# Kernel optimization log

Hardware: AMD Instinct MI355X
Metric: run time of the kernel (lower is better)

Reference implementation:

```python
import jax, jax.numpy as jnp
import numpy as np
from jax import lax

HID = 2048; NK = 16; NV = 32; DK = 128; DV = 128; KSZ = 4; CHUNK = 64; S = 2048
KEY_DIM = NK * DK; VAL_DIM = NV * DV; CONV_DIM = 2 * KEY_DIM + VAL_DIM
EPS = 1e-6


def l2norm(x, eps=1e-6):
    return x * lax.rsqrt((x * x).sum(-1, keepdims=True) + eps)


def chunk_gated_delta_rule(q, k, v, g, beta, chunk=CHUNK):
    # q,k: [B,S,Hv,DK]; v: [B,S,Hv,DV]; g,beta: [B,S,Hv]
    q = l2norm(q); k = l2norm(k)  # use_qk_l2norm_in_kernel=True
    q, k, v = (jnp.swapaxes(x, 1, 2) for x in (q, k, v))  # [B,H,S,D]
    g = jnp.swapaxes(g, 1, 2); beta = jnp.swapaxes(beta, 1, 2)  # [B,H,S]
    B, H, Ssz, Dk = k.shape; Dv = v.shape[-1]
    N = Ssz // chunk  # seq_len chosen divisible by chunk -> pad is no-op
    q = q * (Dk ** -0.5)
    vb = v * beta[..., None]
    kb = k * beta[..., None]
    rs = lambda x: x.reshape(B, H, N, chunk, x.shape[-1])
    q, k, v, kb, vb = map(rs, (q, k, v, kb, vb))
    g = jnp.cumsum(g.reshape(B, H, N, chunk), axis=-1)
    tril = jnp.tril(jnp.ones((chunk, chunk), bool))
    stril = jnp.tril(jnp.ones((chunk, chunk), bool), -1)
    diff = jnp.where(tril, g[..., :, None] - g[..., None, :], 0.0)
    decay_mask = jnp.where(tril, jnp.exp(diff), 0.0)  # [B,H,N,C,C]
    attn = jnp.where(stril, -(kb @ jnp.swapaxes(k, -1, -2)) * decay_mask, 0.0)
    # UT (WY) transform: sequential row updates, scan over in-chunk index
    def ut_body(a, i):
        row = jnp.take(a, i, axis=-2)  # [B,H,N,C]
        new = row + jnp.einsum('bhnk,bhnkj->bhnj', row, a)
        return a.at[:, :, :, i, :].set(new), None
    attn, _ = lax.scan(ut_body, attn, jnp.arange(1, chunk))
    attn = attn + jnp.eye(chunk, dtype=attn.dtype)
    u = attn @ vb                                   # [B,H,N,C,DV]
    kcd = attn @ (kb * jnp.exp(g)[..., None])       # [B,H,N,C,DK]
    init = jnp.zeros((B, H, Dk, Dv), q.dtype)
    def step(state, inp):
        q_i, k_i, u_i, kcd_i, g_i, dm_i = inp
        scores = (q_i @ jnp.swapaxes(k_i, -1, -2)) * dm_i
        v_new = u_i - kcd_i @ state
        inter = (q_i * jnp.exp(g_i)[..., None]) @ state
        o = inter + scores @ v_new
        gl = g_i[..., -1]  # [B,H]
        state = state * jnp.exp(gl)[..., None, None] + jnp.einsum(
            'bhcd,bhce->bhde', k_i * jnp.exp(gl[..., None] - g_i)[..., None], v_new)
        return state, o
    mv = lambda x: jnp.moveaxis(x, 2, 0)
    _, out = lax.scan(step, init, (mv(q), mv(k), mv(u), mv(kcd), mv(g), mv(decay_mask)))
    out = jnp.moveaxis(out, 0, 2).reshape(B, H, Ssz, Dv)
    return jnp.swapaxes(out, 1, 2)  # [B,S,H,DV]


def setup_inputs() -> dict:
    key = jax.random.key(0)
    ks = jax.random.split(key, 8)
    return {
        'hidden_states': jax.random.normal(ks[0], (S, HID), jnp.float32),
        'W_qkv': jax.random.normal(ks[1], (CONV_DIM, HID), jnp.float32) * 0.02,
        'W_z': jax.random.normal(ks[2], (VAL_DIM, HID), jnp.float32) * 0.02,
        'W_a': jax.random.normal(ks[3], (NV, HID), jnp.float32) * 0.02,
        'W_b': jax.random.normal(ks[4], (NV, HID), jnp.float32) * 0.02,
        'conv_w': jax.random.normal(ks[5], (CONV_DIM, 1, KSZ), jnp.float32) * 0.1,
        'dt_bias': jnp.ones((NV,), jnp.float32),
        'A_log': jnp.log(jax.random.uniform(ks[6], (NV,), jnp.float32, 0.1, 16.0)),
        'norm_w': jnp.ones((DV,), jnp.float32),
        'W_out': jax.random.normal(ks[7], (HID, VAL_DIM), jnp.float32) * 0.02,
    }


def reference(hidden_states, W_qkv, W_z, W_a, W_b, conv_w, dt_bias, A_log, norm_w, W_out):
    x = hidden_states  # [S, HID]
    mixed = x @ W_qkv.T  # [S, CONV_DIM]
    z = (x @ W_z.T).reshape(-1, DV)  # [S*NV, DV]
    a = x @ W_a.T  # [S, NV]
    b = x @ W_b.T
    # causal depthwise conv1d (torch pads K-1 both sides then slices [:S])
    conv = lax.conv_general_dilated(
        mixed.T[None], conv_w, (1,), [(KSZ - 1, 0)],
        dimension_numbers=('NCH', 'OIH', 'NCH'), feature_group_count=CONV_DIM)
    mixed = jax.nn.silu(conv[0].T)  # [S, CONV_DIM]
    q = mixed[:, :KEY_DIM].reshape(1, S, NK, DK)
    k = mixed[:, KEY_DIM:2 * KEY_DIM].reshape(1, S, NK, DK)
    v = mixed[:, 2 * KEY_DIM:].reshape(1, S, NV, DV)
    beta = jax.nn.sigmoid(b)[None]  # [1,S,NV]
    g = (-jnp.exp(A_log) * jax.nn.softplus(a + dt_bias))[None]  # [1,S,NV]
    ratio = NV // NK
    q = jnp.repeat(q, ratio, axis=2)
    k = jnp.repeat(k, ratio, axis=2)
    core = chunk_gated_delta_rule(q, k, v, g, beta)  # [1,S,NV,DV]
    h = core.reshape(-1, DV)  # [S*NV, DV]
    var = jnp.mean(h * h, axis=-1, keepdims=True)
    h = h * lax.rsqrt(var + EPS) * norm_w
    h = h * jax.nn.silu(z)
    out = h.reshape(S, VAL_DIM) @ W_out.T  # [S, HID]
    return out
```

## Files before the change

### kernel.cpp

```cpp
#include <hip/hip_runtime.h>
#include <hip/hip_bf16.h>
#include <math.h>

#define S_LEN   2048
#define HIDDIM  2048
#define NKH     16
#define NVH     32
#define DKD     128
#define DVD     128
#define CCH     64
#define NCHK    32
#define KEY_DIM 2048
#define VAL_DIM 4096
#define CONV_DIM 8192

#define PA_LDS_BYTES (16384 + 16384 + 32768 + 4096 + 4096 + 256 + 256 + 256)
#define PB_LDS_BYTES ((8192+8192+4096+8192+2048+1024+1024)*2 + 64*4)
#define G256_LDS_BYTES (3 * 12288 * 2)
#define G128_LDS_BYTES (3 * 8192 * 2)

typedef __bf16 bf16x8 __attribute__((ext_vector_type(8)));
typedef float f32x4 __attribute__((ext_vector_type(4)));

__device__ __forceinline__ float sigmoid_f(float x) { return 1.f / (1.f + __expf(-x)); }
__device__ __forceinline__ float silu_f(float x) { return x * sigmoid_f(x); }
__device__ __forceinline__ ushort f2bf(float f) {
    unsigned u = __float_as_uint(f);
    u += 0x7fffu + ((u >> 16) & 1u);
    return (ushort)(u >> 16);
}
__device__ __forceinline__ float bf2f(ushort u) {
    return __uint_as_float((unsigned)u << 16);
}

#define GLL(srcp, dstp) __builtin_amdgcn_global_load_lds( \
    (const __attribute__((address_space(1))) void*)(srcp), \
    (__attribute__((address_space(3))) void*)(dstp), 16, 0, 0)

__global__ __launch_bounds__(256) void cast_kernel(
    const float* __restrict__ in, ushort* __restrict__ out, int n8)
{
    int t = blockIdx.x * 256 + threadIdx.x;
    if (t >= n8) return;
    float4 v0 = *(const float4*)(in + (size_t)t * 8);
    float4 v1 = *(const float4*)(in + (size_t)t * 8 + 4);
    union { ushort u[8]; uint4 v; } r;
    r.u[0] = f2bf(v0.x); r.u[1] = f2bf(v0.y); r.u[2] = f2bf(v0.z); r.u[3] = f2bf(v0.w);
    r.u[4] = f2bf(v1.x); r.u[5] = f2bf(v1.y); r.u[6] = f2bf(v1.z); r.u[7] = f2bf(v1.w);
    *(uint4*)(out + (size_t)t * 8) = r.v;
}

__global__ __launch_bounds__(256) void cast_ab_kernel(
    const float* __restrict__ Wa, const float* __restrict__ Wb, ushort* __restrict__ out)
{
    int t = blockIdx.x * 256 + threadIdx.x;
    int row = t >> 8;
    int c8 = (t & 255) * 8;
    union { ushort u[8]; uint4 v; } r;
    if (row < 64) {
        const float* src = (row < 32) ? (Wa + (size_t)row * HIDDIM + c8)
                                      : (Wb + (size_t)(row - 32) * HIDDIM + c8);
        float4 v0 = *(const float4*)(src);
        float4 v1 = *(const float4*)(src + 4);
        r.u[0] = f2bf(v0.x); r.u[1] = f2bf(v0.y); r.u[2] = f2bf(v0.z); r.u[3] = f2bf(v0.w);
        r.u[4] = f2bf(v1.x); r.u[5] = f2bf(v1.y); r.u[6] = f2bf(v1.z); r.u[7] = f2bf(v1.w);
    } else {
        r.u[0] = r.u[1] = r.u[2] = r.u[3] = r.u[4] = r.u[5] = r.u[6] = r.u[7] = 0;
    }
    *(uint4*)(out + (size_t)t * 8) = r.v;
}

__global__ __launch_bounds__(512, 2) void gemm256_kernel(
    const ushort* __restrict__ A, const ushort* __restrict__ B,
    float* __restrict__ C0, void* __restrict__ C1,
    int K, int NSPLIT, int ldc0, int ldc1, int c1bf16)
{
    extern __shared__ ushort g2s[];
    const int tid = threadIdx.x;
    const int wv = tid >> 6, ln = tid & 63;
    const int wm = wv >> 2, wn = wv & 3;
    const int lrow = ln & 15, lkg = ln >> 4;
    const int bm = blockIdx.y * 128, bn = blockIdx.x * 256;

    int soffA, soffB[2];
    {
        int l = tid & 63;
        soffA = (((tid >> 6) * 16) + (l & 15)) * K + (l >> 4) * 8;
#pragma unroll
        for (int j = 0; j < 2; ++j) {
            int g = tid + j * 512;
            int lg = g & 63;
            soffB[j] = (((g >> 6) * 16) + (lg & 15)) * K + (lg >> 4) * 8;
        }
    }
    const ushort* Abase = A + (size_t)bm * K;
    const ushort* Bbase = B + (size_t)bn * K;

    f32x4 acc[4][4];
#pragma unroll
    for (int m = 0; m < 4; ++m)
#pragma unroll
        for (int n = 0; n < 4; ++n) {
            f32x4 z = {0.f, 0.f, 0.f, 0.f};
            acc[m][n] = z;
        }

#define G256_STAGE(bb, k0) do {                                            \
        ushort* bufA_ = g2s + (bb) * 12288;                                \
        ushort* bufB_ = bufA_ + 4096;                                      \
        GLL(Abase + soffA + (k0), bufA_ + (wv * 64) * 8);                  \
        _Pragma("unroll")                                                  \
        for (int j_ = 0; j_ < 2; ++j_)                                     \
            GLL(Bbase + soffB[j_] + (k0), bufB_ + (j_ * 512 + wv * 64) * 8);\
    } while (0)

    const int T = K >> 5;
    G256_STAGE(0, 0);
    G256_STAGE(1, 32);
    int bb = 0;
    for (int t = 0; t < T; ++t) {
        if (t + 1 < T) {
            asm volatile("s_waitcnt vmcnt(3)" ::: "memory");
        } else {
            asm volatile("s_waitcnt vmcnt(0)" ::: "memory");
        }
        __builtin_amdgcn_s_barrier();
        if (t + 2 < T) G256_STAGE((bb >= 1) ? (bb - 1) : (bb + 2), (t + 2) * 32);
        const ushort* LA = g2s + bb * 12288;
        const ushort* LB = LA + 4096;
        __builtin_amdgcn_s_setprio(1);
        {
            bf16x8 afv[4], bfv[4];
#pragma unroll
            for (int mf = 0; mf < 4; ++mf)
                afv[mf] = *(const bf16x8*)&LA[((wm * 4 + mf) * 64 + ln) * 8];
#pragma unroll
            for (int nf = 0; nf < 4; ++nf)
                bfv[nf] = *(const bf16x8*)&LB[((wn * 4 + nf) * 64 + ln) * 8];
#pragma unroll
            for (int mf = 0; mf < 4; ++mf)
#pragma unroll
                for (int nf = 0; nf < 4; ++nf)
                    acc[mf][nf] = __builtin_amdgcn_mfma_f32_16x16x32_bf16(
                        afv[mf], bfv[nf], acc[mf][nf], 0, 0, 0);
        }
        __builtin_amdgcn_s_setprio(0);
        bb = (bb == 2) ? 0 : bb + 1;
    }
#undef G256_STAGE

    const bool inC1 = (bn >= NSPLIT);
    const int cboff = bn + wn * 64 - (inC1 ? NSPLIT : 0);
    if (!inC1) {
#pragma unroll
        for (int mf = 0; mf < 4; ++mf) {
            const int row0 = bm + wm * 64 + mf * 16 + lkg * 4;
#pragma unroll
            for (int nf = 0; nf < 4; ++nf) {
                float* cp = C0 + (size_t)row0 * ldc0 + cboff + nf * 16 + lrow;
#pragma unroll
                for (int j = 0; j < 4; ++j) cp[(size_t)j * ldc0] = acc[mf][nf][j];
            }
        }
    } else if (!c1bf16) {
        float* C1f = (float*)C1;
#pragma unroll
        for (int mf = 0; mf < 4; ++mf) {
            const int row0 = bm + wm * 64 + mf * 16 + lkg * 4;
#pragma unroll
            for (int nf = 0; nf < 4; ++nf) {
                float* cp = C1f + (size_t)row0 * ldc1 + cboff + nf * 16 + lrow;
#pragma unroll
                for (int j = 0; j < 4; ++j) cp[(size_t)j * ldc1] = acc[mf][nf][j];
            }
        }
    } else {
        ushort* C1b = (ushort*)C1;
#pragma unroll
        for (int mf = 0; mf < 4; ++mf) {
            const int row0 = bm + wm * 64 + mf * 16 + lkg * 4;
#pragma unroll
            for (int nf = 0; nf < 4; ++nf) {
                ushort* cp = C1b + (size_t)row0 * ldc1 + cboff + nf * 16 + lrow;
#pragma unroll
                for (int j = 0; j < 4; ++j) cp[(size_t)j * ldc1] = f2bf(acc[mf][nf][j]);
            }
        }
    }
}

__global__ __launch_bounds__(256, 2) void gemm128_kernel(
    const ushort* __restrict__ A, const ushort* __restrict__ B,
    float* __restrict__ C, int N, int K)
{
    extern __shared__ ushort g1s[];
    const int tid = threadIdx.x;
    const int wv = tid >> 6, ln = tid & 63;
    const int wm = wv >> 1, wn = wv & 1;
    const int lrow = ln & 15, lkg = ln >> 4;
    const int bm = blockIdx.y * 128, bn = blockIdx.x * 128;

    int soff[2];
#pragma unroll
    for (int j = 0; j < 2; ++j) {
        int g = tid + j * 256;
        int l = g & 63;
        soff[j] = (((g >> 6) * 16) + (l & 15)) * K + (l >> 4) * 8;
    }
    const ushort* Abase = A + (size_t)bm * K;
    const ushort* Bbase = B + (size_t)bn * K;

    f32x4 acc[4][4];
#pragma unroll
    for (int m = 0; m < 4; ++m)
#pragma unroll
        for (int n = 0; n < 4; ++n) {
            f32x4 z = {0.f, 0.f, 0.f, 0.f};
            acc[m][n] = z;
        }

#define G128_STAGE(bb, k0) do {                                            \
        ushort* bufA_ = g1s + (bb) * 8192;                                 \
        ushort* bufB_ = bufA_ + 4096;                                      \
        _Pragma("unroll")                                                  \
        for (int j_ = 0; j_ < 2; ++j_) {                                   \
            GLL(Abase + soff[j_] + (k0), bufA_ + (j_ * 256 + wv * 64) * 8);\
            GLL(Bbase + soff[j_] + (k0), bufB_ + (j_ * 256 + wv * 64) * 8);\
        }                                                                  \
    } while (0)

    const int T = K >> 5;
    G128_STAGE(0, 0);
    G128_STAGE(1, 32);
    int bb = 0;
    for (int t = 0; t < T; ++t) {
        if (t + 1 < T) {
            asm volatile("s_waitcnt vmcnt(4)" ::: "memory");
        } else {
            asm volatile("s_waitcnt vmcnt(0)" ::: "memory");
        }
        __builtin_amdgcn_s_barrier();
        if (t + 2 < T) G128_STAGE((bb >= 1) ? (bb - 1) : (bb + 2), (t + 2) * 32);
        const ushort* LA = g1s + bb * 8192;
        const ushort* LB = LA + 4096;
        __builtin_amdgcn_s_setprio(1);
        {
            bf16x8 afv[4], bfv[4];
#pragma unroll
            for (int mf = 0; mf < 4; ++mf)
                afv[mf] = *(const bf16x8*)&LA[((wm * 4 + mf) * 64 + ln) * 8];
#pragma unroll
            for (int nf = 0; nf < 4; ++nf)
                bfv[nf] = *(const bf16x8*)&LB[((wn * 4 + nf) * 64 + ln) * 8];
#pragma unroll
            for (int mf = 0; mf < 4; ++mf)
#pragma unroll
                for (int nf = 0; nf < 4; ++nf)
                    acc[mf][nf] = __builtin_amdgcn_mfma_f32_16x16x32_bf16(
                        afv[mf], bfv[nf], acc[mf][nf], 0, 0, 0);
        }
        __builtin_amdgcn_s_setprio(0);
        bb = (bb == 2) ? 0 : bb + 1;
    }
#undef G128_STAGE

#pragma unroll
    for (int mf = 0; mf < 4; ++mf) {
        const int row0 = bm + wm * 64 + mf * 16 + lkg * 4;
#pragma unroll
        for (int nf = 0; nf < 4; ++nf) {
            float* cp = C + (size_t)row0 * N + bn + wn * 64 + nf * 16 + lrow;
#pragma unroll
            for (int j = 0; j < 4; ++j) cp[(size_t)j * N] = acc[mf][nf][j];
        }
    }
}

__global__ __launch_bounds__(256) void front_kernel(
    const float* __restrict__ pre, const float* __restrict__ cw,
    ushort* __restrict__ qnb, float* __restrict__ kn, float* __restrict__ vbuf)
{
    __shared__ float stage[4096];
    __shared__ float sums[32];
    __shared__ float scal[32];
    const int s = blockIdx.x;
    const int tid = threadIdx.x;

#pragma unroll
    for (int cg = 0; cg < 8; ++cg) {
        const int c = cg * 1024 + tid * 4;
        float w[4][4];
#pragma unroll
        for (int j = 0; j < 4; ++j) {
            float4 wj = *(const float4*)(cw + (size_t)(c + j) * 4);
            w[j][0] = wj.x; w[j][1] = wj.y; w[j][2] = wj.z; w[j][3] = wj.w;
        }
        float a0 = 0.f, a1 = 0.f, a2 = 0.f, a3 = 0.f;
#pragma unroll
        for (int t = 0; t < 4; ++t) {
            int ss = s - 3 + t;
            if (ss >= 0) {
                float4 x = *(const float4*)(pre + (size_t)ss * CONV_DIM + c);
                a0 = fmaf(x.x, w[0][t], a0);
                a1 = fmaf(x.y, w[1][t], a1);
                a2 = fmaf(x.z, w[2][t], a2);
                a3 = fmaf(x.w, w[3][t], a3);
            }
        }
        a0 = silu_f(a0); a1 = silu_f(a1); a2 = silu_f(a2); a3 = silu_f(a3);
        if (cg < 4) {
            float4 v4 = make_float4(a0, a1, a2, a3);
            *(float4*)&stage[c] = v4;
            float ss2 = a0 * a0 + a1 * a1 + a2 * a2 + a3 * a3;
#pragma unroll
            for (int m = 1; m < 32; m <<= 1) ss2 += __shfl_xor(ss2, m, 32);
            if ((tid & 31) == 0) sums[c >> 7] = ss2;
        } else {
            *(float4*)(vbuf + (size_t)s * VAL_DIM + (c - 4096)) =
                make_float4(a0, a1, a2, a3);
        }
    }
    __syncthreads();
    if (tid < 32) {
        float sc = rsqrtf(sums[tid] + 1e-6f);
        if (tid < 16) sc *= 0.08838834764831843f;
        scal[tid] = sc;
    }
    __syncthreads();
#pragma unroll
    for (int j = 0; j < 4; ++j) {
        const int c = j * 1024 + tid * 4;
        float4 v4 = *(const float4*)&stage[c];
        const float sc = scal[c >> 7];
        v4.x *= sc; v4.y *= sc; v4.z *= sc; v4.w *= sc;
        if (c < 2048) {
            union { ushort u2[4]; uint2 v; } p;
            p.u2[0] = f2bf(v4.x); p.u2[1] = f2bf(v4.y);
            p.u2[2] = f2bf(v4.z); p.u2[3] = f2bf(v4.w);
            *(uint2*)(qnb + ((size_t)(s * NKH + (c >> 7))) * DKD + (c & 127)) = p.v;
        } else {
            *(float4*)(kn + ((size_t)(s * NKH + ((c >> 7) - 16))) * DKD + (c & 127)) = v4;
        }
    }
}

__global__ __launch_bounds__(256) void gb_kernel(
    const float* __restrict__ ab, const float* __restrict__ dt_bias,
    const float* __restrict__ A_log, float* __restrict__ g, float* __restrict__ beta)
{
    int idx = blockIdx.x * 256 + threadIdx.x;
    int s = idx >> 5, h = idx & 31;
    float av = ab[(size_t)s * 128 + h] + dt_bias[h];
    float sp = (av > 20.f) ? av : log1pf(__expf(av));
    g[idx] = -__expf(A_log[h]) * sp;
    beta[idx] = sigmoid_f(ab[(size_t)s * 128 + 32 + h]);
}

__global__ __launch_bounds__(256) void phaseA_kernel(
    const ushort* __restrict__ qnb, const float* __restrict__ kn,
    const float* __restrict__ vbuf, const float* __restrict__ gbuf,
    const float* __restrict__ betabuf,
    float* __restrict__ u, ushort* __restrict__ kcd,
    ushort* __restrict__ scores, float* __restrict__ gcs_out,
    ushort* __restrict__ knT)
{
    extern __shared__ char pasm[];
    ushort* kb    = (ushort*)(pasm);
    ushort* qb    = (ushort*)(pasm + 16384);
    ushort* Xb    = (ushort*)(pasm + 32768);
    float*  Adiag = (float*)(pasm + 65536);
    ushort* Ab    = (ushort*)(pasm + 69632);
    float*  gcs_s = (float*)(pasm + 73728);
    float*  bet_s = (float*)(pasm + 73984);
    float*  scK_s = (float*)(pasm + 74240);
    float*  Pf    = (float*)qb;

    const int n = blockIdx.x, h = blockIdx.y, kh = h >> 1;
    const int tid = threadIdx.x;
    const int s0 = n * CCH;
    const int wv = tid >> 6, ln = tid & 63;
    const int lrow = ln & 15, lkg = ln >> 4;

    float xr[64];
    if (tid < 128) {
        const float* vp = vbuf + (size_t)s0 * VAL_DIM + h * DVD + tid;
#pragma unroll
        for (int i = 0; i < 64; ++i) xr[i] = vp[(size_t)i * VAL_DIM];
    } else {
        const float* kp = kn + ((size_t)s0 * NKH + kh) * DKD + (tid - 128);
#pragma unroll
        for (int i = 0; i < 64; ++i) xr[i] = kp[(size_t)i * (NKH * DKD)];
    }

    {
        uint4 z = {0, 0, 0, 0};
#pragma unroll
        for (int i = 0; i < 8; ++i)
            *(uint4*)&Xb[(i * 256 + tid) * 8] = z;
        *(uint4*)&Ab[tid * 8] = z;
    }

    if (tid < 64) {
        float gv = gbuf[(size_t)(s0 + tid) * NVH + h];
#pragma unroll
        for (int off = 1; off < 64; off <<= 1) {
            float pv = __shfl_up(gv, off, 64);
            if (tid >= off) gv += pv;
        }
        float bv = betabuf[(size_t)(s0 + tid) * NVH + h];
        gcs_s[tid] = gv;
        bet_s[tid] = bv;
        scK_s[tid] = bv * __expf(gv);
        gcs_out[(size_t)h * S_LEN + s0 + tid] = gv;
    }

    {
        const int r = tid >> 2, c0 = (tid & 3) * 32;
        const int mbase = (((r >> 4) * 4 + (tid & 3)) * 64 + (r & 15)) * 8;
        const float* ksrc = kn + ((size_t)(s0 + r) * NKH + kh) * DKD + c0;
#pragma unroll
        for (int j0 = 0; j0 < 4; ++j0) {
            float4 v0 = *(const float4*)(ksrc + j0 * 8);
            float4 v1 = *(const float4*)(ksrc + j0 * 8 + 4);
            union { ushort us[8]; uint4 v; } p;
            p.us[0] = f2bf(v0.x); p.us[1] = f2bf(v0.y); p.us[2] = f2bf(v0.z); p.us[3] = f2bf(v0.w);
            p.us[4] = f2bf(v1.x); p.us[5] = f2bf(v1.y); p.us[6] = f2bf(v1.z); p.us[7] = f2bf(v1.w);
            *(uint4*)&kb[mbase + (j0 << 7)] = p.v;
        }
        const ushort* qsrc = qnb + ((size_t)(s0 + r) * NKH + kh) * DKD + c0;
#pragma unroll
        for (int j0 = 0; j0 < 4; ++j0) {
            uint4 v = *(const uint4*)(qsrc + j0 * 8);
            *(uint4*)&qb[mbase + (j0 << 7)] = v;
        }
    }
    __syncthreads();

    f32x4 accA[4], accQ[4];
#pragma unroll
    for (int j = 0; j < 4; ++j) {
        f32x4 z = {0.f, 0.f, 0.f, 0.f};
        accA[j] = z; accQ[j] = z;
    }
#pragma unroll
    for (int ks = 0; ks < 4; ++ks) {
        bf16x8 a_k = *(const bf16x8*)&kb[((wv * 4 + ks) * 64 + ln) * 8];
        bf16x8 a_q = *(const bf16x8*)&qb[((wv * 4 + ks) * 64 + ln) * 8];
#pragma unroll
        for (int j = 0; j < 4; ++j) {
            bf16x8 b_k = *(const bf16x8*)&kb[((j * 4 + ks) * 64 + ln) * 8];
            accA[j] = __builtin_amdgcn_mfma_f32_16x16x32_bf16(a_k, b_k, accA[j], 0, 0, 0);
            accQ[j] = __builtin_amdgcn_mfma_f32_16x16x32_bf16(a_q, b_k, accQ[j], 0, 0, 0);
        }
    }
    {
        ushort* scp = scores + (size_t)(h * NCHK + n) * (CCH * CCH);
#pragma unroll
        for (int j = 0; j < 4; ++j) {
            const int c = j * 16 + lrow;
            const float gc = gcs_s[c];
#pragma unroll
            for (int jj = 0; jj < 4; ++jj) {
                const int i = wv * 16 + lkg * 4 + jj;
                const float e = __expf(gcs_s[i] - gc);
                float sv = (i >= c) ? (accQ[j][jj] * e) : 0.f;
                scp[i * CCH + c] = f2bf(sv);
                float aval = (i > c) ? (-bet_s[i] * accA[j][jj] * e) : 0.f;
                if (j == wv) {
                    Adiag[wv * 256 + (i & 15) * 16 + lrow] = aval;
                } else if (j < wv) {
                    const int f = (wv == 1) ? 0 : ((wv == 2) ? 1 : (2 + (j >> 1)));
                    const int lk = ((j & 1) << 4) | lrow;
                    const int lane2 = (i & 15) | ((lk >> 3) << 4);
                    Ab[(f * 64 + lane2) * 8 + (lk & 7)] = f2bf(aval);
                }
            }
        }
    }
    if (tid < 128) {
#pragma unroll
        for (int i4 = 0; i4 < 16; ++i4) {
            float4 b4 = *(const float4*)&bet_s[i4 * 4];
            xr[i4 * 4 + 0] *= b4.x; xr[i4 * 4 + 1] *= b4.y;
            xr[i4 * 4 + 2] *= b4.z; xr[i4 * 4 + 3] *= b4.w;
        }
    } else {
#pragma unroll
        for (int i4 = 0; i4 < 16; ++i4) {
            float4 b4 = *(const float4*)&scK_s[i4 * 4];
            xr[i4 * 4 + 0] *= b4.x; xr[i4 * 4 + 1] *= b4.y;
            xr[i4 * 4 + 2] *= b4.z; xr[i4 * 4 + 3] *= b4.w;
        }
    }
    __syncthreads();

    const int ct = tid >> 4, lct = tid & 15;
#pragma unroll
    for (int s = 0; s < 4; ++s) {
        float y[16];
        float pr[16];
        if (s > 0) {
#pragma unroll
            for (int r = 0; r < 16; ++r) pr[r] = Pf[r * 256 + tid];
        } else {
#pragma unroll
            for (int r = 0; r < 16; ++r) pr[r] = 0.f;
        }
#pragma unroll
        for (int r = 0; r < 16; ++r) {
            float acc = xr[s * 16 + r] + pr[r];
#pragma unroll
            for (int k4 = 0; k4 < 16; k4 += 4) {
                if (k4 < r) {
                    float4 a4 = *(const float4*)&Adiag[s * 256 + r * 16 + k4];
                    if (k4 + 0 < r) acc = fmaf(a4.x, y[k4 + 0], acc);
                    if (k4 + 1 < r) acc = fmaf(a4.y, y[k4 + 1], acc);
                    if (k4 + 2 < r) acc = fmaf(a4.z, y[k4 + 2], acc);
                    if (k4 + 3 < r) acc = fmaf(a4.w, y[k4 + 3], acc);
                }
            }
            y[r] = acc;
        }
        if (tid < 128) {
            float* up = u + (size_t)(h * NCHK + n) * (CCH * DVD) + (s * 16) * DVD + tid;
#pragma unroll
            for (int r = 0; r < 16; ++r) up[r * DVD] = y[r];
        } else {
            ushort* kp = kcd + (size_t)(h * NCHK + n) * (CCH * DKD) + (s * 16) * DKD + (tid - 128);
#pragma unroll
            for (int r = 0; r < 16; ++r) kp[r * DKD] = f2bf(y[r]);
        }
        if (s < 3) {
#pragma unroll
            for (int half = 0; half < 2; ++half) {
                union { ushort us[8]; uint4 v; } p;
#pragma unroll
                for (int e = 0; e < 8; ++e) p.us[e] = f2bf(y[half * 8 + e]);
                const int kg = (s & 1) * 2 + half;
                *(uint4*)&Xb[(((s >> 1) * 16 + ct) * 64 + (kg * 16 + lct)) * 8] = p.v;
            }
            __syncthreads();
            const int snx = s + 1;
            const int nT2 = (snx + 1) >> 1;
            f32x4 accP[4];
#pragma unroll
            for (int ctl = 0; ctl < 4; ++ctl) {
                f32x4 z = {0.f, 0.f, 0.f, 0.f};
                accP[ctl] = z;
            }
#pragma unroll
            for (int t2 = 0; t2 < 2; ++t2) {
                if (t2 < nT2) {
                    const int f = (snx == 1) ? 0 : ((snx == 2) ? 1 : (2 + t2));
                    bf16x8 a = *(const bf16x8*)&Ab[(f * 64 + ln) * 8];
#pragma unroll
                    for (int ctl = 0; ctl < 4; ++ctl) {
                        bf16x8 b = *(const bf16x8*)&Xb[((t2 * 16 + wv * 4 + ctl) * 64 + ln) * 8];
                        accP[ctl] = __builtin_amdgcn_mfma_f32_16x16x32_bf16(a, b, accP[ctl], 0, 0, 0);
                    }
                }
            }
#pragma unroll
            for (int ctl = 0; ctl < 4; ++ctl)
#pragma unroll
                for (int jj = 0; jj < 4; ++jj)
                    Pf[(lkg * 4 + jj) * 256 + wv * 64 + ctl * 16 + lrow] = accP[ctl][jj];
            __syncthreads();
        }
    }

    if (!(h & 1)) {
        const int dk = tid >> 1, ch = (tid & 1) * 32;
        ushort* dst = knT + ((size_t)(kh * NCHK + n) * DKD + dk) * CCH + ch;
        const int kpart = ((dk >> 5) * 64) * 8 + (((dk >> 3) & 3) << 4) * 8 + (dk & 7);
#pragma unroll
        for (int j0 = 0; j0 < 32; j0 += 8) {
            union { ushort us[8]; uint4 v; } p;
#pragma unroll
            for (int j = 0; j < 8; ++j) {
                const int row = ch + j0 + j;
                p.us[j] = kb[((row >> 4) * 4 * 64 + (row & 15)) * 8 + kpart];
            }
            *(uint4*)(dst + j0) = p.v;
        }
    }
}

__global__ __launch_bounds__(256) void phaseB_kernel(
    const ushort* __restrict__ qnb, const ushort* __restrict__ knT,
    const float* __restrict__ u, const ushort* __restrict__ kcd,
    const ushort* __restrict__ sc, const float* __restrict__ gcs,
    ushort* __restrict__ obuf)
{
    extern __shared__ ushort smu[];
    ushort* qorg  = smu;
    ushort* kcorg = smu + 8192;
    ushort* scorg = smu + 16384;
    ushort* kTorg = smu + 20480;
    ushort* storg = smu + 28672;
    ushort* vnorg = smu + 30720;
    ushort* vnsorg= smu + 31744;
    float* gcs_s  = (float*)(smu + 32768);

    const int h = blockIdx.x;
    const int dvb = blockIdx.y;
    const int d0 = dvb * 16;
    const int kh = h >> 1;
    const int tid = threadIdx.x;
    const int wv = tid >> 6, ln = tid & 63;
    const int lrow = ln & 15, lkg = ln >> 4;

    for (int i = tid; i < 2048 / 8; i += 256) {
        uint4 z = {0, 0, 0, 0};
        *(uint4*)&storg[i * 8] = z;
    }

    const int q_lane  = lrow * (NKH * DKD) + kh * DKD + wv * 32 + lkg * 8;
    const int kc_lane = lrow * DKD + wv * 32 + lkg * 8;
    const int st_lane = ((tid >> 7) * 16 + lrow) * 64 + ((tid >> 6) & 1) * 32 + lkg * 8;
    const int dst_e   = wv * 512;

    f32x4 accS0 = {0.f, 0.f, 0.f, 0.f}, accS1 = {0.f, 0.f, 0.f, 0.f};

    for (int n = 0; n < NCHK; ++n) {
        const int s0 = n * CCH;
        const ushort* qsrc  = qnb + (size_t)s0 * (NKH * DKD);
        const ushort* kcsrc = kcd + (size_t)(h * NCHK + n) * (CCH * DKD);
        const ushort* scsrc = sc  + (size_t)(h * NCHK + n) * (CCH * CCH);
        const ushort* kTsrc = knT + (size_t)(kh * NCHK + n) * (DKD * CCH);
#pragma unroll
        for (int r = 0; r < 4; ++r) {
            GLL(qsrc + q_lane + r * 32768, &qorg[r * 2048 + dst_e]);
            GLL(kcsrc + kc_lane + r * 2048, &kcorg[r * 2048 + dst_e]);
            GLL(kTsrc + st_lane + r * 2048, &kTorg[r * 2048 + dst_e]);
        }
#pragma unroll
        for (int r = 0; r < 2; ++r)
            GLL(scsrc + st_lane + r * 2048, &scorg[r * 2048 + dst_e]);
        if (tid < 64) gcs_s[tid] = gcs[(size_t)h * S_LEN + s0 + tid];
        __syncthreads();

        f32x4 accv = {0.f, 0.f, 0.f, 0.f};
        f32x4 acco = {0.f, 0.f, 0.f, 0.f};
#pragma unroll
        for (int ks = 0; ks < 4; ++ks) {
            bf16x8 b_st = *(const bf16x8*)&storg[(ks * 64 + ln) * 8];
            bf16x8 a_kc = *(const bf16x8*)&kcorg[((wv * 4 + ks) * 64 + ln) * 8];
            bf16x8 a_q  = *(const bf16x8*)&qorg[((wv * 4 + ks) * 64 + ln) * 8];
            accv = __builtin_amdgcn_mfma_f32_16x16x32_bf16(a_kc, b_st, accv, 0, 0, 0);
            acco = __builtin_amdgcn_mfma_f32_16x16x32_bf16(a_q, b_st, acco, 0, 0, 0);
        }
        const float* up = u + (size_t)(h * NCHK + n) * (CCH * DVD)
                            + (wv * 16 + lkg * 4) * DVD + d0 + lrow;
        float u0 = up[0], u1 = up[DVD], u2 = up[2 * DVD], u3 = up[3 * DVD];
        const float gl = gcs_s[63];
        float vn0 = u0 - accv[0], vn1 = u1 - accv[1];
        float vn2 = u2 - accv[2], vn3 = u3 - accv[3];
        {
            const int row = wv * 16 + lkg * 4;
            float g0 = gcs_s[row], g1 = gcs_s[row + 1], g2 = gcs_s[row + 2], g3 = gcs_s[row + 3];
            acco[0] *= __expf(g0); acco[1] *= __expf(g1);
            acco[2] *= __expf(g2); acco[3] *= __expf(g3);
            const int eb = ((wv >> 1) * 64 + ((wv & 1) * 2 + (lkg >> 1)) * 16 + lrow) * 8
                         + (lkg & 1) * 4;
            union { ushort u2a[4]; uint2 v; } pa, pb;
            pa.u2a[0] = f2bf(vn0); pa.u2a[1] = f2bf(vn1);
            pa.u2a[2] = f2bf(vn2); pa.u2a[3] = f2bf(vn3);
            pb.u2a[0] = f2bf(vn0 * __expf(gl - g0)); pb.u2a[1] = f2bf(vn1 * __expf(gl - g1));
            pb.u2a[2] = f2bf(vn2 * __expf(gl - g2)); pb.u2a[3] = f2bf(vn3 * __expf(gl - g3));
            *(uint2*)&vnorg[eb] = pa.v;
            *(uint2*)&vnsorg[eb] = pb.v;
        }
        __syncthreads();

#pragma unroll
        for (int ks = 0; ks < 2; ++ks) {
            bf16x8 a_sc = *(const bf16x8*)&scorg[((wv * 2 + ks) * 64 + ln) * 8];
            bf16x8 b_vn = *(const bf16x8*)&vnorg[(ks * 64 + ln) * 8];
            acco = __builtin_amdgcn_mfma_f32_16x16x32_bf16(a_sc, b_vn, acco, 0, 0, 0);
        }
        ushort* op = obuf + (size_t)(s0 + wv * 16 + lkg * 4) * VAL_DIM + h * DVD + d0 + lrow;
        op[0] = f2bf(acco[0]); op[VAL_DIM] = f2bf(acco[1]);
        op[2 * VAL_DIM] = f2bf(acco[2]); op[3 * VAL_DIM] = f2bf(acco[3]);

        const float egl = __expf(gl);
        accS0 *= egl; accS1 *= egl;
#pragma unroll
        for (int ks = 0; ks < 2; ++ks) {
            bf16x8 a_vs = *(const bf16x8*)&vnsorg[(ks * 64 + ln) * 8];
            bf16x8 b_k0 = *(const bf16x8*)&kTorg[(((wv * 2 + 0) * 2 + ks) * 64 + ln) * 8];
            bf16x8 b_k1 = *(const bf16x8*)&kTorg[(((wv * 2 + 1) * 2 + ks) * 64 + ln) * 8];
            accS0 = __builtin_amdgcn_mfma_f32_16x16x32_bf16(a_vs, b_k0, accS0, 0, 0, 0);
            accS1 = __builtin_amdgcn_mfma_f32_16x16x32_bf16(a_vs, b_k1, accS1, 0, 0, 0);
        }
#pragma unroll
        for (int j = 0; j < 4; ++j) {
            storg[(wv * 64 + ((lrow >> 3)) * 16 + lkg * 4 + j) * 8 + (lrow & 7)] = f2bf(accS0[j]);
            storg[(wv * 64 + (2 + (lrow >> 3)) * 16 + lkg * 4 + j) * 8 + (lrow & 7)] = f2bf(accS1[j]);
        }
        __syncthreads();
    }
}

__global__ __launch_bounds__(256) void norm_kernel(
    const ushort* __restrict__ obuf, const ushort* __restrict__ z,
    const float* __restrict__ nw, ushort* __restrict__ hbuf)
{
    int row = (blockIdx.x * 256 + threadIdx.x) >> 6;
    int lane = threadIdx.x & 63;
    uint ov = *(const uint*)(obuf + (size_t)row * DVD + lane * 2);
    float x0 = bf2f((ushort)ov), x1 = bf2f((ushort)(ov >> 16));
    float ss = x0 * x0 + x1 * x1;
#pragma unroll
    for (int m = 1; m < 64; m <<= 1) ss += __shfl_xor(ss, m, 64);
    float scale = rsqrtf(ss * (1.f / DVD) + 1e-6f);
    uint zv = *(const uint*)(z + (size_t)row * DVD + lane * 2);
    float z0 = bf2f((ushort)zv), z1 = bf2f((ushort)(zv >> 16));
    float2 w2 = *(const float2*)(nw + lane * 2);
    float h0 = x0 * scale * w2.x * silu_f(z0);
    float h1 = x1 * scale * w2.y * silu_f(z1);
    union { ushort u[2]; uint v; } r;
    r.u[0] = f2bf(h0); r.u[1] = f2bf(h1);
    *(uint*)(hbuf + (size_t)row * DVD + lane * 2) = r.v;
}

extern "C" void kernel_launch(void* const* d_in, const int* in_sizes, int n_in,
                              void* d_out, int out_size, void* d_ws, size_t ws_size,
                              hipStream_t stream)
{
    (void)in_sizes; (void)n_in; (void)out_size; (void)ws_size;
    const float* x      = (const float*)d_in[0];
    const float* W_qkv  = (const float*)d_in[1];
    const float* W_z    = (const float*)d_in[2];
    const float* W_a    = (const float*)d_in[3];
    const float* W_b    = (const float*)d_in[4];
    const float* conv_w = (const float*)d_in[5];
    const float* dt_b   = (const float*)d_in[6];
    const float* A_log  = (const float*)d_in[7];
    const float* norm_w = (const float*)d_in[8];
    const float* W_out  = (const float*)d_in[9];
    float* out = (float*)d_out;

    char* ws = (char*)d_ws;
    float*  mixed_pre = (float*)(ws);
    float*  u_buf     = (float*)(ws);
    ushort* kcd_buf   = (ushort*)(ws + 33554432);
    ushort* knT_buf   = (ushort*)(ws + 50331648);
    ushort* wqz       = (ushort*)(ws + 67108864);
    ushort* xb        = (ushort*)(ws + 117440512);
    float*  vbuf      = (float*)(ws + 67108864);
    ushort* obuf      = (ushort*)(ws + 67108864);
    ushort* hbuf      = (ushort*)(ws + 100663296);
    ushort* wob       = (ushort*)(ws + 117440512);
    ushort* z_buf     = (ushort*)(ws + 134217728);
    ushort* sc_buf    = (ushort*)(ws + 167772160);
    ushort* wabb      = (ushort*)(ws + 167772160);
    float*  ab_buf    = (float*)(ws + 168296448);
    ushort* qnb       = (ushort*)(ws + 176160768);
    float*  kn        = (float*)(ws + 184549376);
    float*  g_buf     = (float*)(ws + 201326592);
    float*  bet_buf   = (float*)(ws + 201588736);
    float*  gcs_buf   = (float*)(ws + 201850880);

    hipFuncSetAttribute((const void*)phaseA_kernel,
                        hipFuncAttributeMaxDynamicSharedMemorySize, PA_LDS_BYTES);
    hipFuncSetAttribute((const void*)phaseB_kernel,
                        hipFuncAttributeMaxDynamicSharedMemorySize, PB_LDS_BYTES);
    hipFuncSetAttribute((const void*)gemm256_kernel,
                        hipFuncAttributeMaxDynamicSharedMemorySize, G256_LDS_BYTES);
    hipFuncSetAttribute((const void*)gemm128_kernel,
                        hipFuncAttributeMaxDynamicSharedMemorySize, G128_LDS_BYTES);

    dim3 blk(256);
    cast_kernel<<<(S_LEN * HIDDIM / 8) / 256, blk, 0, stream>>>(x, xb, S_LEN * HIDDIM / 8);
    cast_kernel<<<(CONV_DIM * HIDDIM / 8) / 256, blk, 0, stream>>>(W_qkv, wqz, CONV_DIM * HIDDIM / 8);
    cast_kernel<<<(VAL_DIM * HIDDIM / 8) / 256, blk, 0, stream>>>(W_z, wqz + (size_t)CONV_DIM * HIDDIM, VAL_DIM * HIDDIM / 8);
    cast_ab_kernel<<<(128 * HIDDIM / 8) / 256, blk, 0, stream>>>(W_a, W_b, wabb);
    gemm256_kernel<<<dim3((CONV_DIM + VAL_DIM) / 256, S_LEN / 128), dim3(512), G256_LDS_BYTES, stream>>>(
        xb, wqz, mixed_pre, (void*)z_buf, HIDDIM, CONV_DIM, CONV_DIM, VAL_DIM, 1);
    gemm128_kernel<<<dim3(1, S_LEN / 128), blk, G128_LDS_BYTES, stream>>>(
        xb, wabb, ab_buf, 128, HIDDIM);
    front_kernel<<<S_LEN, blk, 0, stream>>>(mixed_pre, conv_w, qnb, kn, vbuf);
    gb_kernel<<<(S_LEN * NVH) / 256, blk, 0, stream>>>(ab_buf, dt_b, A_log, g_buf, bet_buf);
    phaseA_kernel<<<dim3(NCHK, NVH), blk, PA_LDS_BYTES, stream>>>(
        qnb, kn, vbuf, g_buf, bet_buf, u_buf, kcd_buf, sc_buf, gcs_buf, knT_buf);
    phaseB_kernel<<<dim3(NVH, 8), blk, PB_LDS_BYTES, stream>>>(
        qnb, knT_buf, u_buf, kcd_buf, sc_buf, gcs_buf, obuf);
    cast_kernel<<<(HIDDIM * VAL_DIM / 8) / 256, blk, 0, stream>>>(W_out, wob, HIDDIM * VAL_DIM / 8);
    norm_kernel<<<(S_LEN * NVH * 64) / 256, blk, 0, stream>>>(obuf, z_buf, norm_w, hbuf);
    gemm128_kernel<<<dim3(HIDDIM / 128, S_LEN / 128), blk, G128_LDS_BYTES, stream>>>(
        hbuf, wob, out, HIDDIM, VAL_DIM);
}
```

Baseline: 478.6 us.

## Double-buffer phaseB chunk loads and store u as bf16 staged in LDS

The sequential phaseB chunk loop gets two LDS buffers, so the global-to-LDS loads for chunk n+1 are issued while chunk n is computed, and the per-chunk load/sync stall goes away. The u intermediate is now written in bf16 instead of fp32, which halves its traffic, and it is staged into LDS with the other operands rather than read directly from global memory. All gcs values for the head are preloaded once. The cost is a much larger LDS footprint per block, which can lower occupancy, plus bf16 rounding of u, which may reduce accuracy.

```diff
diff --git a/kernel.cpp b/kernel.cpp
--- a/kernel.cpp
+++ b/kernel.cpp
@@ -15,7 +15,7 @@
 #define CONV_DIM 8192
 
 #define PA_LDS_BYTES (16384 + 16384 + 32768 + 4096 + 4096 + 256 + 256 + 256)
-#define PB_LDS_BYTES ((8192+8192+4096+8192+2048+1024+1024)*2 + 64*4)
+#define PB_LDS_BYTES ((2 * 29696 + 2048 + 1024 + 1024) * 2 + 2048 * 4)
 #define G256_LDS_BYTES (3 * 12288 * 2)
 #define G128_LDS_BYTES (3 * 8192 * 2)
 
@@ -360,7 +360,7 @@
     const ushort* __restrict__ qnb, const float* __restrict__ kn,
     const float* __restrict__ vbuf, const float* __restrict__ gbuf,
     const float* __restrict__ betabuf,
-    float* __restrict__ u, ushort* __restrict__ kcd,
+    ushort* __restrict__ u, ushort* __restrict__ kcd,
     ushort* __restrict__ scores, float* __restrict__ gcs_out,
     ushort* __restrict__ knT)
 {
@@ -522,9 +522,9 @@
             y[r] = acc;
         }
         if (tid < 128) {
-            float* up = u + (size_t)(h * NCHK + n) * (CCH * DVD) + (s * 16) * DVD + tid;
-#pragma unroll
-            for (int r = 0; r < 16; ++r) up[r * DVD] = y[r];
+            ushort* up = u + (size_t)(h * NCHK + n) * (CCH * DVD) + (s * 16) * DVD + tid;
+#pragma unroll
+            for (int r = 0; r < 16; ++r) up[r * DVD] = f2bf(y[r]);
         } else {
             ushort* kp = kcd + (size_t)(h * NCHK + n) * (CCH * DKD) + (s * 16) * DKD + (tid - 128);
 #pragma unroll
@@ -588,19 +588,15 @@
 
 __global__ __launch_bounds__(256) void phaseB_kernel(
     const ushort* __restrict__ qnb, const ushort* __restrict__ knT,
-    const float* __restrict__ u, const ushort* __restrict__ kcd,
+    const ushort* __restrict__ u, const ushort* __restrict__ kcd,
     const ushort* __restrict__ sc, const float* __restrict__ gcs,
     ushort* __restrict__ obuf)
 {
     extern __shared__ ushort smu[];
-    ushort* qorg  = smu;
-    ushort* kcorg = smu + 8192;
-    ushort* scorg = smu + 16384;
-    ushort* kTorg = smu + 20480;
-    ushort* storg = smu + 28672;
-    ushort* vnorg = smu + 30720;
-    ushort* vnsorg= smu + 31744;
-    float* gcs_s  = (float*)(smu + 32768);
+    ushort* storg  = smu + 59392;
+    ushort* vnorg  = smu + 61440;
+    ushort* vnsorg = smu + 62464;
+    float*  gcsall = (float*)(smu + 63488);
 
     const int h = blockIdx.x;
     const int dvb = blockIdx.y;
@@ -610,9 +606,9 @@
     const int wv = tid >> 6, ln = tid & 63;
     const int lrow = ln & 15, lkg = ln >> 4;
 
-    for (int i = tid; i < 2048 / 8; i += 256) {
+    {
         uint4 z = {0, 0, 0, 0};
-        *(uint4*)&storg[i * 8] = z;
+        *(uint4*)&storg[tid * 8] = z;
     }
 
     const int q_lane  = lrow * (NKH * DKD) + kh * DKD + wv * 32 + lkg * 8;
@@ -620,25 +616,47 @@
     const int st_lane = ((tid >> 7) * 16 + lrow) * 64 + ((tid >> 6) & 1) * 32 + lkg * 8;
     const int dst_e   = wv * 512;
 
+#define PBSTG(bsel, nn) do {                                                  \
+        const ushort* qsrc_  = qnb + (size_t)((nn) * CCH) * (NKH * DKD);      \
+        const ushort* kcsrc_ = kcd + (size_t)(h * NCHK + (nn)) * (CCH * DKD); \
+        const ushort* scsrc_ = sc  + (size_t)(h * NCHK + (nn)) * (CCH * CCH); \
+        const ushort* kTsrc_ = knT + (size_t)(kh * NCHK + (nn)) * (DKD * CCH);\
+        const ushort* usrc_  = u   + (size_t)(h * NCHK + (nn)) * (CCH * DVD) + d0; \
+        ushort* base_ = smu + (bsel) * 29696;                                 \
+        _Pragma("unroll")                                                     \
+        for (int r_ = 0; r_ < 4; ++r_) {                                      \
+            GLL(qsrc_ + q_lane + r_ * 32768, base_ + r_ * 2048 + dst_e);      \
+            GLL(kcsrc_ + kc_lane + r_ * 2048, base_ + 8192 + r_ * 2048 + dst_e); \
+            GLL(kTsrc_ + st_lane + r_ * 2048, base_ + 20480 + r_ * 2048 + dst_e); \
+        }                                                                     \
+        _Pragma("unroll")                                                     \
+        for (int r_ = 0; r_ < 2; ++r_)                                        \
+            GLL(scsrc_ + st_lane + r_ * 2048, base_ + 16384 + r_ * 2048 + dst_e); \
+        if (tid < 128)                                                        \
+            GLL(usrc_ + (tid >> 1) * DVD + (tid & 1) * 8, base_ + 28672 + tid * 8); \
+    } while (0)
+
+    PBSTG(0, 0);
+    {
+        float4 g0 = *(const float4*)(gcs + (size_t)h * S_LEN + tid * 8);
+        float4 g1 = *(const float4*)(gcs + (size_t)h * S_LEN + tid * 8 + 4);
+        *(float4*)&gcsall[tid * 8] = g0;
+        *(float4*)&gcsall[tid * 8 + 4] = g1;
+    }
+    __syncthreads();
+
     f32x4 accS0 = {0.f, 0.f, 0.f, 0.f}, accS1 = {0.f, 0.f, 0.f, 0.f};
 
     for (int n = 0; n < NCHK; ++n) {
+        const int cur = n & 1;
+        if (n + 1 < NCHK) PBSTG(cur ^ 1, n + 1);
+        const ushort* qorg  = smu + cur * 29696;
+        const ushort* kcorg = qorg + 8192;
+        const ushort* scorg = qorg + 16384;
+        const ushort* kTorg = qorg + 20480;
+        const ushort* uorg  = qorg + 28672;
+        const float*  gcs_s = gcsall + n * 64;
         const int s0 = n * CCH;
-        const ushort* qsrc  = qnb + (size_t)s0 * (NKH * DKD);
-        const ushort* kcsrc = kcd + (size_t)(h * NCHK + n) * (CCH * DKD);
-        const ushort* scsrc = sc  + (size_t)(h * NCHK + n) * (CCH * CCH);
-        const ushort* kTsrc = knT + (size_t)(kh * NCHK + n) * (DKD * CCH);
-#pragma unroll
-        for (int r = 0; r < 4; ++r) {
-            GLL(qsrc + q_lane + r * 32768, &qorg[r * 2048 + dst_e]);
-            GLL(kcsrc + kc_lane + r * 2048, &kcorg[r * 2048 + dst_e]);
-            GLL(kTsrc + st_lane + r * 2048, &kTorg[r * 2048 + dst_e]);
-        }
-#pragma unroll
-        for (int r = 0; r < 2; ++r)
-            GLL(scsrc + st_lane + r * 2048, &scorg[r * 2048 + dst_e]);
-        if (tid < 64) gcs_s[tid] = gcs[(size_t)h * S_LEN + s0 + tid];
-        __syncthreads();
 
         f32x4 accv = {0.f, 0.f, 0.f, 0.f};
         f32x4 acco = {0.f, 0.f, 0.f, 0.f};
@@ -650,14 +668,15 @@
             accv = __builtin_amdgcn_mfma_f32_16x16x32_bf16(a_kc, b_st, accv, 0, 0, 0);
             acco = __builtin_amdgcn_mfma_f32_16x16x32_bf16(a_q, b_st, acco, 0, 0, 0);
         }
-        const float* up = u + (size_t)(h * NCHK + n) * (CCH * DVD)
-                            + (wv * 16 + lkg * 4) * DVD + d0 + lrow;
-        float u0 = up[0], u1 = up[DVD], u2 = up[2 * DVD], u3 = up[3 * DVD];
+        const int row = wv * 16 + lkg * 4;
+        float u0 = bf2f(uorg[(row + 0) * 16 + lrow]);
+        float u1 = bf2f(uorg[(row + 1) * 16 + lrow]);
+        float u2 = bf2f(uorg[(row + 2) * 16 + lrow]);
+        float u3 = bf2f(uorg[(row + 3) * 16 + lrow]);
         const float gl = gcs_s[63];
         float vn0 = u0 - accv[0], vn1 = u1 - accv[1];
         float vn2 = u2 - accv[2], vn3 = u3 - accv[3];
         {
-            const int row = wv * 16 + lkg * 4;
             float g0 = gcs_s[row], g1 = gcs_s[row + 1], g2 = gcs_s[row + 2], g3 = gcs_s[row + 3];
             acco[0] *= __expf(g0); acco[1] *= __expf(g1);
             acco[2] *= __expf(g2); acco[3] *= __expf(g3);
@@ -679,7 +698,7 @@
             bf16x8 b_vn = *(const bf16x8*)&vnorg[(ks * 64 + ln) * 8];
             acco = __builtin_amdgcn_mfma_f32_16x16x32_bf16(a_sc, b_vn, acco, 0, 0, 0);
         }
-        ushort* op = obuf + (size_t)(s0 + wv * 16 + lkg * 4) * VAL_DIM + h * DVD + d0 + lrow;
+        ushort* op = obuf + (size_t)(s0 + row) * VAL_DIM + h * DVD + d0 + lrow;
         op[0] = f2bf(acco[0]); op[VAL_DIM] = f2bf(acco[1]);
         op[2 * VAL_DIM] = f2bf(acco[2]); op[3 * VAL_DIM] = f2bf(acco[3]);
 
@@ -700,6 +719,7 @@
         }
         __syncthreads();
     }
+#undef PBSTG
 }
 
 __global__ __launch_bounds__(256) void norm_kernel(
@@ -743,7 +763,7 @@
 
     char* ws = (char*)d_ws;
     float*  mixed_pre = (float*)(ws);
-    float*  u_buf     = (float*)(ws);
+    ushort* u_buf     = (ushort*)(ws);
     ushort* kcd_buf   = (ushort*)(ws + 33554432);
     ushort* knT_buf   = (ushort*)(ws + 50331648);
     ushort* wqz       = (ushort*)(ws + 67108864);
```

New measurement: 467.7 us. 2.3% less time.
